# Performance work log

Measured on AMD Instinct MI355X. Metric: run time of the kernel, lower is better.

Reference implementation:

```python
import jax, jax.numpy as jnp
import numpy as np

B, N, C, H = 4, 2048, 768, 12


def setup_inputs() -> dict:
    key = jax.random.key(0)
    k1, k2, k3 = jax.random.split(key, 3)
    x = jax.random.normal(k1, (B, N, C), dtype=jnp.float32)
    qkv_w = jax.random.normal(k2, (3 * C, C), dtype=jnp.float32) * 0.02
    proj_w = jax.random.normal(k3, (C, C), dtype=jnp.float32) * 0.02
    proj_b = jnp.zeros((C,), dtype=jnp.float32)
    return {"x": x, "qkv_w": qkv_w, "proj_w": proj_w, "proj_b": proj_b}


def reference(x, qkv_w, proj_w, proj_b):
    b, n, c = x.shape
    hd = c // H
    scale = hd ** -0.5
    # qkv projection (no bias): (B,N,3C) -> (3,B,H,N,hd)
    qkv = (x @ qkv_w.T).reshape(b, n, 3, H, hd).transpose(2, 0, 3, 1, 4)
    q = qkv[0] * scale
    k = qkv[1]
    v = qkv[2]
    attn = jax.nn.softmax(jnp.einsum('bhqd,bhkd->bhqk', q, k), axis=-1)
    out = jnp.einsum('bhqk,bhkd->bhqd', attn, v)  # (B,H,N,hd)
    out = out.transpose(0, 2, 1, 3).reshape(b, n, c)
    return out @ proj_w.T + proj_b
```

## Files before the change

### kernel.cpp

```cpp
#include <hip/hip_runtime.h>

#define B_SZ 4
#define SEQ  2048
#define CH   768
#define NH   12
#define HD   64

typedef float f32x4  __attribute__((ext_vector_type(4)));
typedef __bf16 bf16x8 __attribute__((ext_vector_type(8)));
typedef __bf16 bf16x2 __attribute__((ext_vector_type(2)));

#define MFMA16(a,b,c) __builtin_amdgcn_mfma_f32_16x16x32_bf16(a,b,c,0,0,0)

#define QSCALE 0.1803368801111204f

#if __has_builtin(__builtin_amdgcn_exp2f)
#define EXP2(x) __builtin_amdgcn_exp2f(x)
#else
#define EXP2(x) exp2f(x)
#endif

#define SWZ(row) (((row) ^ ((row) >> 3)) & 7)

__device__ __forceinline__ unsigned pack2(float a, float b) {
    union { bf16x2 v; unsigned u; } p;
    p.v[0] = (__bf16)a; p.v[1] = (__bf16)b;
    return p.u;
}

__device__ __forceinline__ void lds_dma16(const void* g, void* l) {
    __builtin_amdgcn_global_load_lds(
        (const __attribute__((address_space(1))) void*)g,
        (__attribute__((address_space(3))) void*)(unsigned)(unsigned long long)l,
        16, 0, 0);
}

__global__ __launch_bounds__(256) void convert_bf16(const float* __restrict__ src,
                                                    __bf16* __restrict__ dst, int n) {
    int i = (blockIdx.x * 256 + threadIdx.x) * 4;
    if (i >= n) return;
    float4 v = *(const float4*)(src + i);
    union { __bf16 h[4]; uint2 u; } o;
    o.h[0] = (__bf16)v.x; o.h[1] = (__bf16)v.y; o.h[2] = (__bf16)v.z; o.h[3] = (__bf16)v.w;
    *(uint2*)(dst + i) = o.u;
}

__device__ __forceinline__ void gemm128_loop(const __bf16* __restrict__ A,
                                             const __bf16* __restrict__ Bm,
                                             int K, int rowBlk, int colBlk,
                                             __bf16* As, __bf16* Bs,
                                             f32x4 acc[4][4]) {
    const int tid  = threadIdx.x;
    const int lane = tid & 63, wid = tid >> 6;
    const int quad = lane >> 4, l16 = lane & 15;
    const int wm = wid >> 1, wn = wid & 1;

    f32x4 z = {0.f, 0.f, 0.f, 0.f};
#pragma unroll
    for (int mi = 0; mi < 4; ++mi)
#pragma unroll
        for (int ni = 0; ni < 4; ++ni) acc[mi][ni] = z;

    for (int k0 = 0; k0 < K; k0 += 64) {
        __syncthreads();
#pragma unroll
        for (int i = 0; i < 4; ++i) {
            int s = i * 256 + tid;
            int row = s >> 3, pc = s & 7;
            int lc = pc ^ (row & 7);
            lds_dma16(A  + (size_t)(rowBlk + row) * K + k0 + lc * 8, As + s * 8);
            lds_dma16(Bm + (size_t)(colBlk + row) * K + k0 + lc * 8, Bs + s * 8);
        }
        __syncthreads();

#pragma unroll
        for (int kc = 0; kc < 2; ++kc) {
            bf16x8 af[4], bfr[4];
#pragma unroll
            for (int mi = 0; mi < 4; ++mi) {
                int row = wm * 64 + mi * 16 + l16;
                int pc = (quad + 4 * kc) ^ (row & 7);
                af[mi] = *(const bf16x8*)(As + row * 64 + pc * 8);
            }
#pragma unroll
            for (int ni = 0; ni < 4; ++ni) {
                int row = wn * 64 + ni * 16 + l16;
                int pc = (quad + 4 * kc) ^ (row & 7);
                bfr[ni] = *(const bf16x8*)(Bs + row * 64 + pc * 8);
            }
#pragma unroll
            for (int mi = 0; mi < 4; ++mi)
#pragma unroll
                for (int ni = 0; ni < 4; ++ni)
                    acc[mi][ni] = MFMA16(af[mi], bfr[ni], acc[mi][ni]);
        }
    }
}

__global__ __launch_bounds__(256) void qkv_gemm(const __bf16* __restrict__ Xb,
                                                const __bf16* __restrict__ Wb,
                                                __bf16* __restrict__ Qb,
                                                __bf16* __restrict__ Kb,
                                                __bf16* __restrict__ Vt) {
    __shared__ __bf16 smem[128 * 128];
    f32x4 acc[4][4];
    const int rowBlk = blockIdx.x * 128, colBlk = blockIdx.y * 128;
    gemm128_loop(Xb, Wb, CH, rowBlk, colBlk, smem, smem + 128 * 64, acc);

    const int tid = threadIdx.x;
    const int lane = tid & 63, wid = tid >> 6;
    const int quad = lane >> 4, l16 = lane & 15, wm = wid >> 1, wn = wid & 1;
    const int b = rowBlk >> 11, n0 = rowBlk & (SEQ - 1);

    if (colBlk < 2 * CH) {
        const int isK = (colBlk >= CH);
#pragma unroll
        for (int mi = 0; mi < 4; ++mi)
#pragma unroll
            for (int ni = 0; ni < 4; ++ni)
#pragma unroll
                for (int r = 0; r < 4; ++r) {
                    int n = n0 + wm * 64 + mi * 16 + quad * 4 + r;
                    int cc = colBlk - (isK ? CH : 0) + wn * 64 + ni * 16 + l16;
                    int h = cc >> 6, d = cc & 63;
                    size_t idx = (size_t)((b * NH + h) * SEQ + n) * HD + d;
                    float v = acc[mi][ni][r];
                    if (isK) Kb[idx] = (__bf16)v;
                    else     Qb[idx] = (__bf16)(v * QSCALE);
                }
    } else {
        const int vblk = colBlk - 2 * CH;
        __syncthreads();
#pragma unroll
        for (int mi = 0; mi < 4; ++mi)
#pragma unroll
            for (int ni = 0; ni < 4; ++ni)
#pragma unroll
                for (int r = 0; r < 4; ++r) {
                    int rl = wm * 64 + mi * 16 + quad * 4 + r;
                    int cl = wn * 64 + ni * 16 + l16;
                    smem[cl * 128 + (((rl >> 3) ^ (cl & 15)) << 3) + (rl & 7)] =
                        (__bf16)acc[mi][ni][r];
                }
        __syncthreads();
        const int dl = tid >> 1;
        const int d  = vblk + dl;
        const int h  = d >> 6, dd = d & 63;
        const size_t base = (size_t)((b * NH + h) * HD + dd) * SEQ + n0;
#pragma unroll
        for (int j2 = 0; j2 < 8; ++j2) {
            int j = (tid & 1) * 8 + j2;
            uint4 val = *(const uint4*)(smem + dl * 128 + ((j ^ (dl & 15)) << 3));
            *(uint4*)(Vt + base + j * 8) = val;
        }
    }
}

__global__ __launch_bounds__(256, 3) void flash_attn(const __bf16* __restrict__ Qb,
                                                     const __bf16* __restrict__ Kb,
                                                     const __bf16* __restrict__ Vt,
                                                     __bf16* __restrict__ Ab) {
    __shared__ __bf16 smem[9216];
    __bf16* Ks = smem;
    __bf16* Vs = smem + 4096;

    const int tid  = threadIdx.x;
    const int lane = tid & 63, wid = tid >> 6;
    const int quad = lane >> 4, l16 = lane & 15;

    const int lin  = blockIdx.x;
    const int xcd  = lin & 7, idx = lin >> 3;
    const int bh   = xcd * 6 + (idx >> 4);
    const int qblk = idx & 15;
    const int b    = bh / NH, head = bh - b * NH;

    const int qA = qblk * 128 + wid * 16 + l16;
    const int qB = qA + 64;

    bf16x8 qfA[2], qfB[2];
#pragma unroll
    for (int kcd = 0; kcd < 2; ++kcd) {
        qfA[kcd] = *(const bf16x8*)(Qb + (size_t)(bh * SEQ + qA) * HD + kcd * 32 + quad * 8);
        qfB[kcd] = *(const bf16x8*)(Qb + (size_t)(bh * SEQ + qB) * HD + kcd * 32 + quad * 8);
    }

    const int key_e = ((l16 >> 2) << 3) + (l16 & 3);
    const int key_o = ((((l16 >> 2) ^ 1)) << 3) + 4 + (l16 & 3);

    f32x4 otA[4], otB[4];
    f32x4 z = {0.f, 0.f, 0.f, 0.f};
#pragma unroll
    for (int dg = 0; dg < 4; ++dg) { otA[dg] = z; otB[dg] = z; }
    float lA = 0.f, lB = 0.f;

    const __bf16* Kbh = Kb + (size_t)bh * SEQ * HD;
    const __bf16* Vbh = Vt + (size_t)bh * HD * SEQ;

    const int s_row = tid >> 3, s_pc = tid & 7;
    const int s_lc0 = s_pc ^ SWZ(s_row);
    const int s_lc1 = s_pc ^ SWZ(s_row + 32);

    for (int kb = 0; kb < SEQ / 64; ++kb) {
        const int kbase = kb * 64;
        __syncthreads();
        lds_dma16(Kbh + (size_t)(kbase + s_row) * HD + s_lc0 * 8,       Ks + tid * 8);
        lds_dma16(Kbh + (size_t)(kbase + s_row + 32) * HD + s_lc1 * 8,  Ks + 2048 + tid * 8);
        lds_dma16(Vbh + (size_t)s_row * SEQ + kbase + s_lc0 * 8,        Vs + tid * 8);
        lds_dma16(Vbh + (size_t)(s_row + 32) * SEQ + kbase + s_lc1 * 8, Vs + 2048 + tid * 8);
        __syncthreads();

        f32x4 stA[4], stB[4];
#pragma unroll
        for (int g = 0; g < 4; ++g) { stA[g] = z; stB[g] = z; }
#pragma unroll
        for (int g = 0; g < 4; ++g) {
            const int key = ((g >> 1) << 5) + ((g & 1) ? key_o : key_e);
#pragma unroll
            for (int kcd = 0; kcd < 2; ++kcd) {
                int c8 = quad + (kcd << 2);
                bf16x8 kf = *(const bf16x8*)(Ks + key * 64 + ((c8 ^ SWZ(key)) << 3));
                stA[g] = MFMA16(kf, qfA[kcd], stA[g]);
                stB[g] = MFMA16(kf, qfB[kcd], stB[g]);
            }
        }

        bf16x8 pfA[2], pfB[2];
#pragma unroll
        for (int g = 0; g < 4; ++g)
#pragma unroll
            for (int r = 0; r < 4; ++r) {
                float p = EXP2(stA[g][r]);
                stA[g][r] = p;
                lA += p;
            }
#pragma unroll
        for (int kk = 0; kk < 2; ++kk) {
            unsigned w0 = pack2(stA[2 * kk][0], stA[2 * kk][1]);
            unsigned w1 = pack2(stA[2 * kk][2], stA[2 * kk][3]);
            unsigned x0 = pack2(stA[2 * kk + 1][0], stA[2 * kk + 1][1]);
            unsigned x1 = pack2(stA[2 * kk + 1][2], stA[2 * kk + 1][3]);
            unsigned w2 = (unsigned)__shfl_xor((int)x0, 16, 64);
            unsigned w3 = (unsigned)__shfl_xor((int)x1, 16, 64);
            union { bf16x8 v; unsigned u[4]; } f;
            f.u[0] = w0; f.u[1] = w1; f.u[2] = w2; f.u[3] = w3;
            pfA[kk] = f.v;
        }
#pragma unroll
        for (int g = 0; g < 4; ++g)
#pragma unroll
            for (int r = 0; r < 4; ++r) {
                float p = EXP2(stB[g][r]);
                stB[g][r] = p;
                lB += p;
            }
#pragma unroll
        for (int kk = 0; kk < 2; ++kk) {
            unsigned w0 = pack2(stB[2 * kk][0], stB[2 * kk][1]);
            unsigned w1 = pack2(stB[2 * kk][2], stB[2 * kk][3]);
            unsigned x0 = pack2(stB[2 * kk + 1][0], stB[2 * kk + 1][1]);
            unsigned x1 = pack2(stB[2 * kk + 1][2], stB[2 * kk + 1][3]);
            unsigned w2 = (unsigned)__shfl_xor((int)x0, 16, 64);
            unsigned w3 = (unsigned)__shfl_xor((int)x1, 16, 64);
            union { bf16x8 v; unsigned u[4]; } f;
            f.u[0] = w0; f.u[1] = w1; f.u[2] = w2; f.u[3] = w3;
            pfB[kk] = f.v;
        }

#pragma unroll
        for (int dg = 0; dg < 4; ++dg)
#pragma unroll
            for (int kk = 0; kk < 2; ++kk) {
                int row = (dg << 4) + l16;
                int c8 = quad + (kk << 2);
                bf16x8 vf = *(const bf16x8*)(Vs + row * 64 + ((c8 ^ SWZ(row)) << 3));
                otA[dg] = MFMA16(vf, pfA[kk], otA[dg]);
                otB[dg] = MFMA16(vf, pfB[kk], otB[dg]);
            }
    }

    lA += __shfl_xor(lA, 16, 64);
    lA += __shfl_xor(lA, 32, 64);
    lB += __shfl_xor(lB, 16, 64);
    lB += __shfl_xor(lB, 32, 64);
    const float rA = 1.f / lA, rB = 1.f / lB;

    __syncthreads();
    __bf16 (*Ob)[72] = (__bf16(*)[72])smem;
#pragma unroll
    for (int dg = 0; dg < 4; ++dg)
#pragma unroll
        for (int r = 0; r < 4; ++r) {
            int d = (dg << 4) + (quad << 2) + r;
            Ob[wid * 16 + l16][d]      = (__bf16)(otA[dg][r] * rA);
            Ob[64 + wid * 16 + l16][d] = (__bf16)(otB[dg][r] * rB);
        }
    __syncthreads();
    {
        const int row = tid >> 1, c0 = (tid & 1) * 32;
        __bf16* dst = Ab + (size_t)(b * SEQ + qblk * 128 + row) * CH + head * HD + c0;
#pragma unroll
        for (int j = 0; j < 4; ++j)
            *(uint4*)(dst + j * 8) = *(const uint4*)(&Ob[row][c0 + j * 8]);
    }
}

__global__ __launch_bounds__(256) void proj_gemm(const __bf16* __restrict__ Ab,
                                                 const __bf16* __restrict__ Pw,
                                                 const float* __restrict__ bias,
                                                 float* __restrict__ out) {
    __shared__ __bf16 As[128 * 64];
    __shared__ __bf16 Bs[128 * 64];
    f32x4 acc[4][4];
    const int rowBlk = blockIdx.x * 128, colBlk = blockIdx.y * 128;
    gemm128_loop(Ab, Pw, CH, rowBlk, colBlk, As, Bs, acc);

    const int lane = threadIdx.x & 63, wid = threadIdx.x >> 6;
    const int quad = lane >> 4, l16 = lane & 15, wm = wid >> 1, wn = wid & 1;
#pragma unroll
    for (int mi = 0; mi < 4; ++mi)
#pragma unroll
        for (int ni = 0; ni < 4; ++ni)
#pragma unroll
            for (int r = 0; r < 4; ++r) {
                int row = rowBlk + wm * 64 + mi * 16 + quad * 4 + r;
                int col = colBlk + wn * 64 + ni * 16 + l16;
                out[(size_t)row * CH + col] = acc[mi][ni][r] + bias[col];
            }
}

extern "C" void kernel_launch(void* const* d_in, const int* in_sizes, int n_in,
                              void* d_out, int out_size, void* d_ws, size_t ws_size,
                              hipStream_t stream) {
    const float* x      = (const float*)d_in[0];
    const float* qkv_w  = (const float*)d_in[1];
    const float* proj_w = (const float*)d_in[2];
    const float* proj_b = (const float*)d_in[3];
    float* out = (float*)d_out;

    char* ws = (char*)d_ws;
    const size_t nX = (size_t)B_SZ * SEQ * CH;
    const size_t nW = (size_t)3 * CH * CH;
    const size_t nP = (size_t)CH * CH;
    const size_t nQ = (size_t)B_SZ * NH * SEQ * HD;

    __bf16* Xb = (__bf16*)(ws);
    __bf16* Wb = (__bf16*)(ws + 2 * nX);
    __bf16* Pw = (__bf16*)(ws + 2 * (nX + nW));
    __bf16* Qb = (__bf16*)(ws + 2 * (nX + nW + nP));
    __bf16* Kb = (__bf16*)(ws + 2 * (nX + nW + nP + nQ));
    __bf16* Vt = (__bf16*)(ws + 2 * (nX + nW + nP + 2 * nQ));
    __bf16* Ab = (__bf16*)(ws + 2 * (nX + nW + nP + 3 * nQ));

    convert_bf16<<<(int)(nX / 1024), 256, 0, stream>>>(x, Xb, (int)nX);
    convert_bf16<<<(int)(nW / 1024), 256, 0, stream>>>(qkv_w, Wb, (int)nW);
    convert_bf16<<<(int)(nP / 1024), 256, 0, stream>>>(proj_w, Pw, (int)nP);

    qkv_gemm<<<dim3((B_SZ * SEQ) / 128, (3 * CH) / 128), 256, 0, stream>>>(Xb, Wb, Qb, Kb, Vt);

    flash_attn<<<768, 256, 0, stream>>>(Qb, Kb, Vt, Ab);

    proj_gemm<<<dim3((B_SZ * SEQ) / 128, CH / 128), 256, 0, stream>>>(Ab, Pw, proj_b, out);
}
```

Measured before the change: 215.5 us.

## Merge bf16 conversion launches and load 128-key tiles per attention iteration

The three fp32-to-bf16 conversion kernels are fused into one launch that dispatches on block index, removing two kernel launches. The flash-attention loop now stages 128 keys of K and V per iteration (two 64-key halves) and processes both between a single pair of barriers. This halves the number of barrier syncs and iterations. In exchange LDS use per block rises from about 18 KB to 32 KB, which may reduce occupancy against the launch bounds of 3 blocks per SM. The convert kernel also drops its bounds check, which is safe only because the sizes divide exactly.

```diff
diff --git a/kernel.cpp b/kernel.cpp
--- a/kernel.cpp
+++ b/kernel.cpp
@@ -35,10 +35,23 @@
         16, 0, 0);
 }
 
-__global__ __launch_bounds__(256) void convert_bf16(const float* __restrict__ src,
-                                                    __bf16* __restrict__ dst, int n) {
-    int i = (blockIdx.x * 256 + threadIdx.x) * 4;
-    if (i >= n) return;
+#define NBLK_X  6144
+#define NBLK_W  1728
+#define NBLK_P   576
+__global__ __launch_bounds__(256) void convert_all(const float* __restrict__ x,
+                                                   const float* __restrict__ w,
+                                                   const float* __restrict__ p,
+                                                   __bf16* __restrict__ ox,
+                                                   __bf16* __restrict__ ow,
+                                                   __bf16* __restrict__ op) {
+    int blk = blockIdx.x;
+    const float* src;
+    __bf16* dst;
+    int base;
+    if (blk < NBLK_X)               { src = x; dst = ox; base = blk; }
+    else if (blk < NBLK_X + NBLK_W) { src = w; dst = ow; base = blk - NBLK_X; }
+    else                            { src = p; dst = op; base = blk - NBLK_X - NBLK_W; }
+    int i = (base * 256 + threadIdx.x) * 4;
     float4 v = *(const float4*)(src + i);
     union { __bf16 h[4]; uint2 u; } o;
     o.h[0] = (__bf16)v.x; o.h[1] = (__bf16)v.y; o.h[2] = (__bf16)v.z; o.h[3] = (__bf16)v.w;
@@ -160,9 +173,7 @@
                                                      const __bf16* __restrict__ Kb,
                                                      const __bf16* __restrict__ Vt,
                                                      __bf16* __restrict__ Ab) {
-    __shared__ __bf16 smem[9216];
-    __bf16* Ks = smem;
-    __bf16* Vs = smem + 4096;
+    __shared__ __bf16 smem[16384];
 
     const int tid  = threadIdx.x;
     const int lane = tid & 63, wid = tid >> 6;
@@ -200,83 +211,92 @@
     const int s_lc0 = s_pc ^ SWZ(s_row);
     const int s_lc1 = s_pc ^ SWZ(s_row + 32);
 
-    for (int kb = 0; kb < SEQ / 64; ++kb) {
-        const int kbase = kb * 64;
-        __syncthreads();
-        lds_dma16(Kbh + (size_t)(kbase + s_row) * HD + s_lc0 * 8,       Ks + tid * 8);
-        lds_dma16(Kbh + (size_t)(kbase + s_row + 32) * HD + s_lc1 * 8,  Ks + 2048 + tid * 8);
-        lds_dma16(Vbh + (size_t)s_row * SEQ + kbase + s_lc0 * 8,        Vs + tid * 8);
-        lds_dma16(Vbh + (size_t)(s_row + 32) * SEQ + kbase + s_lc1 * 8, Vs + 2048 + tid * 8);
-        __syncthreads();
-
-        f32x4 stA[4], stB[4];
-#pragma unroll
-        for (int g = 0; g < 4; ++g) { stA[g] = z; stB[g] = z; }
-#pragma unroll
-        for (int g = 0; g < 4; ++g) {
-            const int key = ((g >> 1) << 5) + ((g & 1) ? key_o : key_e);
-#pragma unroll
-            for (int kcd = 0; kcd < 2; ++kcd) {
-                int c8 = quad + (kcd << 2);
-                bf16x8 kf = *(const bf16x8*)(Ks + key * 64 + ((c8 ^ SWZ(key)) << 3));
-                stA[g] = MFMA16(kf, qfA[kcd], stA[g]);
-                stB[g] = MFMA16(kf, qfB[kcd], stB[g]);
-            }
-        }
-
-        bf16x8 pfA[2], pfB[2];
-#pragma unroll
-        for (int g = 0; g < 4; ++g)
-#pragma unroll
-            for (int r = 0; r < 4; ++r) {
-                float p = EXP2(stA[g][r]);
-                stA[g][r] = p;
-                lA += p;
-            }
-#pragma unroll
-        for (int kk = 0; kk < 2; ++kk) {
-            unsigned w0 = pack2(stA[2 * kk][0], stA[2 * kk][1]);
-            unsigned w1 = pack2(stA[2 * kk][2], stA[2 * kk][3]);
-            unsigned x0 = pack2(stA[2 * kk + 1][0], stA[2 * kk + 1][1]);
-            unsigned x1 = pack2(stA[2 * kk + 1][2], stA[2 * kk + 1][3]);
-            unsigned w2 = (unsigned)__shfl_xor((int)x0, 16, 64);
-            unsigned w3 = (unsigned)__shfl_xor((int)x1, 16, 64);
-            union { bf16x8 v; unsigned u[4]; } f;
-            f.u[0] = w0; f.u[1] = w1; f.u[2] = w2; f.u[3] = w3;
-            pfA[kk] = f.v;
-        }
-#pragma unroll
-        for (int g = 0; g < 4; ++g)
-#pragma unroll
-            for (int r = 0; r < 4; ++r) {
-                float p = EXP2(stB[g][r]);
-                stB[g][r] = p;
-                lB += p;
-            }
-#pragma unroll
-        for (int kk = 0; kk < 2; ++kk) {
-            unsigned w0 = pack2(stB[2 * kk][0], stB[2 * kk][1]);
-            unsigned w1 = pack2(stB[2 * kk][2], stB[2 * kk][3]);
-            unsigned x0 = pack2(stB[2 * kk + 1][0], stB[2 * kk + 1][1]);
-            unsigned x1 = pack2(stB[2 * kk + 1][2], stB[2 * kk + 1][3]);
-            unsigned w2 = (unsigned)__shfl_xor((int)x0, 16, 64);
-            unsigned w3 = (unsigned)__shfl_xor((int)x1, 16, 64);
-            union { bf16x8 v; unsigned u[4]; } f;
-            f.u[0] = w0; f.u[1] = w1; f.u[2] = w2; f.u[3] = w3;
-            pfB[kk] = f.v;
-        }
-
-#pragma unroll
-        for (int dg = 0; dg < 4; ++dg)
-#pragma unroll
-            for (int kk = 0; kk < 2; ++kk) {
-                int row = (dg << 4) + l16;
-                int c8 = quad + (kk << 2);
-                bf16x8 vf = *(const bf16x8*)(Vs + row * 64 + ((c8 ^ SWZ(row)) << 3));
-                otA[dg] = MFMA16(vf, pfA[kk], otA[dg]);
-                otB[dg] = MFMA16(vf, pfB[kk], otB[dg]);
-            }
-    }
+#define PROCESS(Ks, Vs)                                                                       \
+    do {                                                                                      \
+        f32x4 stA[4], stB[4];                                                                 \
+        _Pragma("unroll")                                                                     \
+        for (int g = 0; g < 4; ++g) { stA[g] = z; stB[g] = z; }                               \
+        _Pragma("unroll")                                                                     \
+        for (int g = 0; g < 4; ++g) {                                                         \
+            const int key = ((g >> 1) << 5) + ((g & 1) ? key_o : key_e);                      \
+            _Pragma("unroll")                                                                 \
+            for (int kcd = 0; kcd < 2; ++kcd) {                                               \
+                int c8 = quad + (kcd << 2);                                                   \
+                bf16x8 kf = *(const bf16x8*)((Ks) + key * 64 + ((c8 ^ SWZ(key)) << 3));       \
+                stA[g] = MFMA16(kf, qfA[kcd], stA[g]);                                        \
+                stB[g] = MFMA16(kf, qfB[kcd], stB[g]);                                        \
+            }                                                                                 \
+        }                                                                                     \
+        bf16x8 pfA[2], pfB[2];                                                                \
+        _Pragma("unroll")                                                                     \
+        for (int g = 0; g < 4; ++g)                                                           \
+            _Pragma("unroll")                                                                 \
+            for (int r = 0; r < 4; ++r) {                                                     \
+                float p = EXP2(stA[g][r]);                                                    \
+                stA[g][r] = p;                                                                \
+                lA += p;                                                                      \
+            }                                                                                 \
+        _Pragma("unroll")                                                                     \
+        for (int kk = 0; kk < 2; ++kk) {                                                      \
+            unsigned w0 = pack2(stA[2 * kk][0], stA[2 * kk][1]);                              \
+            unsigned w1 = pack2(stA[2 * kk][2], stA[2 * kk][3]);                              \
+            unsigned x0 = pack2(stA[2 * kk + 1][0], stA[2 * kk + 1][1]);                      \
+            unsigned x1 = pack2(stA[2 * kk + 1][2], stA[2 * kk + 1][3]);                      \
+            unsigned w2 = (unsigned)__shfl_xor((int)x0, 16, 64);                              \
+            unsigned w3 = (unsigned)__shfl_xor((int)x1, 16, 64);                              \
+            union { bf16x8 v; unsigned u[4]; } f;                                             \
+            f.u[0] = w0; f.u[1] = w1; f.u[2] = w2; f.u[3] = w3;                               \
+            pfA[kk] = f.v;                                                                    \
+        }                                                                                     \
+        _Pragma("unroll")                                                                     \
+        for (int g = 0; g < 4; ++g)                                                           \
+            _Pragma("unroll")                                                                 \
+            for (int r = 0; r < 4; ++r) {                                                     \
+                float p = EXP2(stB[g][r]);                                                    \
+                stB[g][r] = p;                                                                \
+                lB += p;                                                                      \
+            }                                                                                 \
+        _Pragma("unroll")                                                                     \
+        for (int kk = 0; kk < 2; ++kk) {                                                      \
+            unsigned w0 = pack2(stB[2 * kk][0], stB[2 * kk][1]);                              \
+            unsigned w1 = pack2(stB[2 * kk][2], stB[2 * kk][3]);                              \
+            unsigned x0 = pack2(stB[2 * kk + 1][0], stB[2 * kk + 1][1]);                      \
+            unsigned x1 = pack2(stB[2 * kk + 1][2], stB[2 * kk + 1][3]);                      \
+            unsigned w2 = (unsigned)__shfl_xor((int)x0, 16, 64);                              \
+            unsigned w3 = (unsigned)__shfl_xor((int)x1, 16, 64);                              \
+            union { bf16x8 v; unsigned u[4]; } f;                                             \
+            f.u[0] = w0; f.u[1] = w1; f.u[2] = w2; f.u[3] = w3;                               \
+            pfB[kk] = f.v;                                                                    \
+        }                                                                                     \
+        _Pragma("unroll")                                                                     \
+        for (int dg = 0; dg < 4; ++dg)                                                        \
+            _Pragma("unroll")                                                                 \
+            for (int kk = 0; kk < 2; ++kk) {                                                  \
+                int row = (dg << 4) + l16;                                                    \
+                int c8 = quad + (kk << 2);                                                    \
+                bf16x8 vf = *(const bf16x8*)((Vs) + row * 64 + ((c8 ^ SWZ(row)) << 3));       \
+                otA[dg] = MFMA16(vf, pfA[kk], otA[dg]);                                       \
+                otB[dg] = MFMA16(vf, pfB[kk], otB[dg]);                                       \
+            }                                                                                 \
+    } while (0)
+
+    for (int kb = 0; kb < SEQ / 128; ++kb) {
+        const int kbase = kb * 128;
+        __syncthreads();
+        lds_dma16(Kbh + (size_t)(kbase + s_row) * HD + s_lc0 * 8,            smem + tid * 8);
+        lds_dma16(Kbh + (size_t)(kbase + s_row + 32) * HD + s_lc1 * 8,       smem + 2048 + tid * 8);
+        lds_dma16(Vbh + (size_t)s_row * SEQ + kbase + s_lc0 * 8,             smem + 4096 + tid * 8);
+        lds_dma16(Vbh + (size_t)(s_row + 32) * SEQ + kbase + s_lc1 * 8,      smem + 6144 + tid * 8);
+        lds_dma16(Kbh + (size_t)(kbase + 64 + s_row) * HD + s_lc0 * 8,       smem + 8192 + tid * 8);
+        lds_dma16(Kbh + (size_t)(kbase + 96 + s_row) * HD + s_lc1 * 8,       smem + 10240 + tid * 8);
+        lds_dma16(Vbh + (size_t)s_row * SEQ + kbase + 64 + s_lc0 * 8,        smem + 12288 + tid * 8);
+        lds_dma16(Vbh + (size_t)(s_row + 32) * SEQ + kbase + 64 + s_lc1 * 8, smem + 14336 + tid * 8);
+        __syncthreads();
+
+        PROCESS(smem, smem + 4096);
+        PROCESS(smem + 8192, smem + 12288);
+    }
+#undef PROCESS
 
     lA += __shfl_xor(lA, 16, 64);
     lA += __shfl_xor(lA, 32, 64);
@@ -351,9 +371,7 @@
     __bf16* Vt = (__bf16*)(ws + 2 * (nX + nW + nP + 2 * nQ));
     __bf16* Ab = (__bf16*)(ws + 2 * (nX + nW + nP + 3 * nQ));
 
-    convert_bf16<<<(int)(nX / 1024), 256, 0, stream>>>(x, Xb, (int)nX);
-    convert_bf16<<<(int)(nW / 1024), 256, 0, stream>>>(qkv_w, Wb, (int)nW);
-    convert_bf16<<<(int)(nP / 1024), 256, 0, stream>>>(proj_w, Pw, (int)nP);
+    convert_all<<<NBLK_X + NBLK_W + NBLK_P, 256, 0, stream>>>(x, qkv_w, proj_w, Xb, Wb, Pw);
 
     qkv_gemm<<<dim3((B_SZ * SEQ) / 128, (3 * CH) / 128), 256, 0, stream>>>(Xb, Wb, Qb, Kb, Vt);
 
```

Measured after the change: 210.3 us. 1.03x faster.
